# Optimization experiments

Measured on AMD Instinct MI355X. Metric: run time of the kernel, lower is better.

Reference implementation:

```python
import jax, jax.numpy as jnp
import numpy as np
from jax import lax

D_MODEL = 1024
D_STATE = 16
EXPAND = 2
KERNEL = 4
BATCH = 4
SEQ = 4096
LN_EPS = 1e-5


def _ln(x, w, b):
    m = jnp.mean(x, axis=-1, keepdims=True)
    v = jnp.mean((x - m) ** 2, axis=-1, keepdims=True)
    return (x - m) * lax.rsqrt(v + LN_EPS) * w + b


def setup_inputs() -> dict:
    key = jax.random.key(0)
    ks = jax.random.split(key, 16)
    d, n, e, k = D_MODEL, D_STATE, EXPAND, KERNEL

    def lin(key, fan_in, shape):
        bound = 1.0 / np.sqrt(fan_in)
        return jax.random.uniform(key, shape, jnp.float32, -bound, bound)

    return {
        "x": jax.random.normal(ks[0], (BATCH, SEQ, d), jnp.float32),
        "ln1_w": jnp.ones((d,), jnp.float32),
        "ln1_b": jnp.zeros((d,), jnp.float32),
        "conv_w": lin(ks[1], k, (d, 1, k)),  # depthwise conv, groups=d -> fan_in=k
        "conv_b": lin(ks[2], k, (d,)),
        "lns_w": jnp.ones((d,), jnp.float32),
        "lns_b": jnp.zeros((d,), jnp.float32),
        "in_w": lin(ks[3], d, (d, 2 * d)),
        "in_b": lin(ks[4], d, (2 * d,)),
        "xp_w": lin(ks[5], d, (d, n)),
        "xp_b": lin(ks[6], d, (n,)),
        "A_log": jax.random.normal(ks[7], (n,), jnp.float32),
        "D": jax.random.normal(ks[8], (n, d), jnp.float32),
        "out_w": lin(ks[9], d, (d, d)),
        "out_b": lin(ks[10], d, (d,)),
        "ln2_w": jnp.ones((d,), jnp.float32),
        "ln2_b": jnp.zeros((d,), jnp.float32),
        "mlp_w1": lin(ks[11], d, (d, e * d)),
        "mlp_b1": lin(ks[12], d, (e * d,)),
        "mlp_w2": lin(ks[13], e * d, (e * d, d)),
        "mlp_b2": lin(ks[14], e * d, (d,)),
    }


def reference(x, ln1_w, ln1_b, conv_w, conv_b, lns_w, lns_b, in_w, in_b,
              xp_w, xp_b, A_log, D, out_w, out_b, ln2_w, ln2_b,
              mlp_w1, mlp_b1, mlp_w2, mlp_b2):
    b, s, d = x.shape
    # --- depthwise causal-padded conv branch (truncated to seq_len) ---
    xn = _ln(x, ln1_w, ln1_b)
    xc = jnp.transpose(xn, (0, 2, 1))  # (b, d, s)
    xc = lax.conv_general_dilated(
        xc, conv_w, window_strides=(1,), padding=[(KERNEL - 1, KERNEL - 1)],
        feature_group_count=d, dimension_numbers=("NCH", "OIH", "NCH"))
    xc = xc + conv_b[None, :, None]
    xc = jnp.transpose(xc, (0, 2, 1))[:, :s]  # (b, s, d)
    x = x + xc

    # --- SelectiveScanLayer ---
    residual = x
    xn = _ln(x, lns_w, lns_b)
    xz = xn @ in_w + in_b
    xp, z = jnp.split(xz, 2, axis=-1)
    xp = jax.nn.silu(xp)
    z = jax.nn.sigmoid(z)
    u = xp @ xp_w + xp_b  # (b, s, n)
    decay = jnp.exp(-jnp.exp(A_log))  # exp(A), A = -exp(A_log); (n,)

    u_t = jnp.transpose(u, (1, 0, 2))  # (s, b, n)

    def step(h, u_i):
        h = decay * h + u_i
        return h, h

    _, hs = lax.scan(step, jnp.zeros((b, D_STATE), x.dtype), u_t)  # (s, b, n)
    ys = jnp.einsum("sbn,nd->sbd", hs, D) * jnp.transpose(z, (1, 0, 2))
    ys = ys @ out_w + out_b  # (s, b, d)
    # faithful to original: torch stack gives (1,s,b,d), then .view(b,s,d)
    y = ys.reshape(b, s, d)
    x = residual + y

    # --- MLP (dropout inactive at eval) ---
    h = _ln(x, ln2_w, ln2_b)
    h = jax.nn.gelu(h @ mlp_w1 + mlp_b1, approximate=False)
    h = h @ mlp_w2 + mlp_b2
    return x + h
```

## Files before the change

kernel.cpp:

```cpp
#include <hip/hip_runtime.h>
#include <cstdint>
#include <cstddef>


typedef short bf16x8 __attribute__((ext_vector_type(8)));
typedef float f32x4 __attribute__((ext_vector_type(4)));

#define GLD16(gp, lp)                                                          \
  __builtin_amdgcn_global_load_lds(                                            \
      (__attribute__((address_space(1))) void*)(gp),                           \
      (__attribute__((address_space(3))) void*)(lp), 16, 0, 0)

static __device__ __forceinline__ ushort f2bf(float f) {
  union { float f; uint32_t u; } c; c.f = f;
  uint32_t r = c.u + 0x7FFFu + ((c.u >> 16) & 1u);
  return (ushort)(r >> 16);
}
static __device__ __forceinline__ float bf2f(ushort u) {
  union { uint32_t u; float f; } c; c.u = ((uint32_t)u) << 16;
  return c.f;
}

template <int BF16OUT>
__global__ __launch_bounds__(256) void ln_kernel(
    const float* __restrict__ x, const float* __restrict__ w,
    const float* __restrict__ b, void* __restrict__ out) {
  const int row = blockIdx.x;
  const int tid = threadIdx.x;
  const float4 v = ((const float4*)(x + (size_t)row * 1024))[tid];
  float s  = v.x + v.y + v.z + v.w;
  float s2 = v.x * v.x + v.y * v.y + v.z * v.z + v.w * v.w;
#pragma unroll
  for (int off = 32; off > 0; off >>= 1) {
    s  += __shfl_down(s, off);
    s2 += __shfl_down(s2, off);
  }
  __shared__ float red[8];
  const int wv = tid >> 6, ln = tid & 63;
  if (ln == 0) { red[wv] = s; red[4 + wv] = s2; }
  __syncthreads();
  s  = red[0] + red[1] + red[2] + red[3];
  s2 = red[4] + red[5] + red[6] + red[7];
  const float mean = s * (1.f / 1024.f);
  const float var  = s2 * (1.f / 1024.f) - mean * mean;
  const float rstd = rsqrtf(var + 1e-5f);
  const float4 wv4 = ((const float4*)w)[tid];
  const float4 bv4 = ((const float4*)b)[tid];
  const float o0 = (v.x - mean) * rstd * wv4.x + bv4.x;
  const float o1 = (v.y - mean) * rstd * wv4.y + bv4.y;
  const float o2 = (v.z - mean) * rstd * wv4.z + bv4.z;
  const float o3 = (v.w - mean) * rstd * wv4.w + bv4.w;
  if (BF16OUT) {
    ushort4 o; o.x = f2bf(o0); o.y = f2bf(o1); o.z = f2bf(o2); o.w = f2bf(o3);
    ((ushort4*)((ushort*)out + (size_t)row * 1024))[tid] = o;
  } else {
    float4 o; o.x = o0; o.y = o1; o.z = o2; o.w = o3;
    ((float4*)((float*)out + (size_t)row * 1024))[tid] = o;
  }
}

__global__ __launch_bounds__(256) void lnconv_kernel(
    const float* __restrict__ x, const float* __restrict__ ln1w,
    const float* __restrict__ ln1b, const float* __restrict__ cw,
    const float* __restrict__ cb, const float* __restrict__ lnsw,
    const float* __restrict__ lnsb, float* __restrict__ x1,
    ushort* __restrict__ abuf) {
  const int row = blockIdx.x;
  const int t = row & 4095;
  const int tid = threadIdx.x;
  const int wv = tid >> 6, ln = tid & 63;
  const float4* x4 = (const float4*)x;
  float4 xr[4];
  float s[4], q[4];
#pragma unroll
  for (int j = 0; j < 4; j++) {
    const int tt = t - 3 + j;
    if (tt >= 0)
      xr[j] = x4[(size_t)(row - 3 + j) * 256 + tid];
    else
      xr[j] = make_float4(0.f, 0.f, 0.f, 0.f);
    s[j] = xr[j].x + xr[j].y + xr[j].z + xr[j].w;
    q[j] = xr[j].x * xr[j].x + xr[j].y * xr[j].y + xr[j].z * xr[j].z +
           xr[j].w * xr[j].w;
  }
#pragma unroll
  for (int off = 32; off > 0; off >>= 1) {
#pragma unroll
    for (int j = 0; j < 4; j++) {
      s[j] += __shfl_down(s[j], off);
      q[j] += __shfl_down(q[j], off);
    }
  }
  __shared__ float red[4][8];
  __shared__ float red2[8];
  if (ln == 0) {
#pragma unroll
    for (int j = 0; j < 4; j++) { red[wv][j] = s[j]; red[wv][4 + j] = q[j]; }
  }
  __syncthreads();
  float4 wv4 = ((const float4*)ln1w)[tid];
  float4 bv4 = ((const float4*)ln1b)[tid];
  const int c0 = tid * 4;
  float4 acc = *(const float4*)(cb + c0);
  const float4 w0 = *(const float4*)(cw + (size_t)(c0 + 0) * 4);
  const float4 w1 = *(const float4*)(cw + (size_t)(c0 + 1) * 4);
  const float4 w2 = *(const float4*)(cw + (size_t)(c0 + 2) * 4);
  const float4 w3 = *(const float4*)(cw + (size_t)(c0 + 3) * 4);
#pragma unroll
  for (int j = 0; j < 4; j++) {
    if (t - 3 + j >= 0) {
      const float sm = red[0][j] + red[1][j] + red[2][j] + red[3][j];
      const float sq = red[0][4 + j] + red[1][4 + j] + red[2][4 + j] +
                       red[3][4 + j];
      const float mean = sm * (1.f / 1024.f);
      const float var  = sq * (1.f / 1024.f) - mean * mean;
      const float rstd = rsqrtf(var + 1e-5f);
      const float lx = (xr[j].x - mean) * rstd * wv4.x + bv4.x;
      const float ly = (xr[j].y - mean) * rstd * wv4.y + bv4.y;
      const float lz = (xr[j].z - mean) * rstd * wv4.z + bv4.z;
      const float lw = (xr[j].w - mean) * rstd * wv4.w + bv4.w;
      acc.x += lx * ((const float*)&w0)[j];
      acc.y += ly * ((const float*)&w1)[j];
      acc.z += lz * ((const float*)&w2)[j];
      acc.w += lw * ((const float*)&w3)[j];
    }
  }
  float4 o;
  o.x = xr[3].x + acc.x; o.y = xr[3].y + acc.y;
  o.z = xr[3].z + acc.z; o.w = xr[3].w + acc.w;
  ((float4*)x1)[(size_t)row * 256 + tid] = o;
  float s2 = o.x + o.y + o.z + o.w;
  float q2 = o.x * o.x + o.y * o.y + o.z * o.z + o.w * o.w;
#pragma unroll
  for (int off = 32; off > 0; off >>= 1) {
    s2 += __shfl_down(s2, off);
    q2 += __shfl_down(q2, off);
  }
  if (ln == 0) { red2[wv] = s2; red2[4 + wv] = q2; }
  __syncthreads();
  const float sm = red2[0] + red2[1] + red2[2] + red2[3];
  const float sq = red2[4] + red2[5] + red2[6] + red2[7];
  const float mean = sm * (1.f / 1024.f);
  const float var  = sq * (1.f / 1024.f) - mean * mean;
  const float rstd = rsqrtf(var + 1e-5f);
  wv4 = ((const float4*)lnsw)[tid];
  bv4 = ((const float4*)lnsb)[tid];
  ushort4 a;
  a.x = f2bf((o.x - mean) * rstd * wv4.x + bv4.x);
  a.y = f2bf((o.y - mean) * rstd * wv4.y + bv4.y);
  a.z = f2bf((o.z - mean) * rstd * wv4.z + bv4.z);
  a.w = f2bf((o.w - mean) * rstd * wv4.w + bv4.w);
  ((ushort4*)(abuf + (size_t)row * 1024))[tid] = a;
}

__global__ __launch_bounds__(256) void wt_all_kernel(
    const float* __restrict__ in_w, const float* __restrict__ out_w,
    const float* __restrict__ w1, const float* __restrict__ w2,
    ushort* __restrict__ in_wT, ushort* __restrict__ out_wT,
    ushort* __restrict__ w1T, ushort* __restrict__ w2T) {
  __shared__ float tile[32][33];
  const int idx = blockIdx.x;
  const float* src; ushort* dst; int K, N, n0, k0;
  if (idx < 2048) {
    src = in_w; dst = in_wT; K = 1024; N = 2048;
    n0 = (idx & 63) * 32; k0 = (idx >> 6) * 32;
  } else if (idx < 3072) {
    const int r = idx - 2048;
    src = out_w; dst = out_wT; K = 1024; N = 1024;
    n0 = (r & 31) * 32; k0 = (r >> 5) * 32;
  } else if (idx < 5120) {
    const int r = idx - 3072;
    src = w1; dst = w1T; K = 1024; N = 2048;
    n0 = (r & 63) * 32; k0 = (r >> 6) * 32;
  } else {
    const int r = idx - 5120;
    src = w2; dst = w2T; K = 2048; N = 1024;
    n0 = (r & 31) * 32; k0 = (r >> 5) * 32;
  }
  const int tx = threadIdx.x & 31, ty = threadIdx.x >> 5;
#pragma unroll
  for (int j = 0; j < 32; j += 8)
    tile[ty + j][tx] = src[(size_t)(k0 + ty + j) * N + n0 + tx];
  __syncthreads();
#pragma unroll
  for (int j = 0; j < 32; j += 8)
    dst[(size_t)(n0 + ty + j) * K + k0 + tx] = f2bf(tile[tx][ty + j]);
}

__global__ __launch_bounds__(256) void u_mfma_kernel(
    const ushort* __restrict__ xp, const float* __restrict__ xpw,
    const float* __restrict__ xpb, float* __restrict__ u) {
  __shared__ ushort Ws[16 * 1024];
  __shared__ ushort As[64 * 64];
  const int tid = threadIdx.x;
  const int wave = tid >> 6, lane = tid & 63;
  const int l16 = lane & 15, quad = lane >> 4;
  for (int e = tid; e < 16384; e += 256) {
    const int n = e & 15, k = e >> 4;
    Ws[n * 1024 + (((k >> 3) ^ (n & 7)) << 3) + (k & 7)] =
        f2bf(xpw[(size_t)k * 16 + n]);
  }
  const int bm0 = blockIdx.x * 64;
  const int srow = lane >> 3, sblk = (lane & 7) ^ (srow & 7);
  const ushort* Ag = xp + (size_t)(bm0 + wave * 16 + srow) * 1024 + sblk * 8;
  ushort* Al = &As[wave * 16 * 64];
  const int rsw = l16 & 7;
  f32x4 acc = (f32x4){0.f, 0.f, 0.f, 0.f};
  __syncthreads();
  for (int k0 = 0; k0 < 1024; k0 += 64) {
    GLD16(Ag + k0, Al);
    GLD16(Ag + k0 + (size_t)8 * 1024, Al + 512);
    __syncthreads();
#pragma unroll
    for (int kh = 0; kh < 2; kh++) {
      const bf16x8 aF = *(const bf16x8*)
          &As[(wave * 16 + l16) * 64 + (((kh * 4 + quad) ^ rsw) << 3)];
      const bf16x8 bF = *(const bf16x8*)
          &Ws[l16 * 1024 + ((((k0 >> 3) + kh * 4 + quad) ^ rsw) << 3)];
      acc = __builtin_amdgcn_mfma_f32_16x16x32_bf16(aF, bF, acc, 0, 0, 0);
    }
    __syncthreads();
  }
  const float bv = xpb[l16];
#pragma unroll
  for (int r = 0; r < 4; r++) {
    const int row = bm0 + wave * 16 + quad * 4 + r;
    u[(size_t)row * 16 + l16] = acc[r] + bv;
  }
}

__global__ __launch_bounds__(256) void scan_kernel(
    const float* __restrict__ u, const float* __restrict__ A_log,
    float* __restrict__ hs) {
  const int tid = threadIdx.x;
  const int b = blockIdx.x >> 4;
  const int n = blockIdx.x & 15;
  const float d = expf(-expf(A_log[n]));
  const int t0 = tid * 16;
  const float* up = u + ((size_t)b * 4096) * 16 + n;
  float loc[16];
  float h = 0.f;
#pragma unroll
  for (int i = 0; i < 16; i++) {
    h = d * h + up[(size_t)(t0 + i) * 16];
    loc[i] = h;
  }
  __shared__ float sv[256];
  sv[tid] = h;
  __syncthreads();
  float d16 = d * d; d16 *= d16; d16 *= d16; d16 *= d16;
  float f = d16;
  for (int off = 1; off < 256; off <<= 1) {
    const float add = (tid >= off) ? sv[tid - off] : 0.f;
    __syncthreads();
    sv[tid] += f * add;
    __syncthreads();
    f *= f;
  }
  const float carry = (tid > 0) ? sv[tid - 1] : 0.f;
  float dp = d;
#pragma unroll
  for (int i = 0; i < 16; i++) {
    const float hg = loc[i] + dp * carry;
    dp *= d;
    hs[((size_t)(t0 + i) * 4 + b) * 16 + n] = hg;
  }
}

__global__ __launch_bounds__(256) void g_kernel(
    const float* __restrict__ hs, const float* __restrict__ Dm,
    const ushort* __restrict__ z, ushort* __restrict__ g) {
  __shared__ float hsh[256];
  const int tid = threadIdx.x;
  const int r0 = blockIdx.x * 16;
  hsh[tid] = hs[(size_t)r0 * 16 + tid];
  __syncthreads();
  float4 acc[16];
#pragma unroll
  for (int rr = 0; rr < 16; rr++) acc[rr] = make_float4(0.f, 0.f, 0.f, 0.f);
  const float4* Dv = (const float4*)Dm;
#pragma unroll
  for (int n = 0; n < 16; n++) {
    const float4 dv = Dv[(size_t)n * 256 + tid];
#pragma unroll
    for (int rr = 0; rr < 16; rr++) {
      const float h = hsh[rr * 16 + n];
      acc[rr].x += h * dv.x; acc[rr].y += h * dv.y;
      acc[rr].z += h * dv.z; acc[rr].w += h * dv.w;
    }
  }
#pragma unroll
  for (int rr = 0; rr < 16; rr++) {
    const int r = r0 + rr;
    const int b = r & 3, t = r >> 2;
    const ushort4 zv =
        *(const ushort4*)(z + ((size_t)b * 4096 + t) * 1024 + tid * 4);
    ushort4 o;
    o.x = f2bf(acc[rr].x * bf2f(zv.x)); o.y = f2bf(acc[rr].y * bf2f(zv.y));
    o.z = f2bf(acc[rr].z * bf2f(zv.z)); o.w = f2bf(acc[rr].w * bf2f(zv.w));
    *(ushort4*)(g + (size_t)r * 1024 + tid * 4) = o;
  }
}

template <int EPI>
__global__ __launch_bounds__(256) void gemm_bt(
    const ushort* __restrict__ A, const ushort* __restrict__ Bt,
    const float* __restrict__ bias, int K, void* __restrict__ p0,
    void* __restrict__ p1) {
  __shared__ ushort As[2][128 * 32];
  __shared__ ushort Bs[2][128 * 32];
  const int tid = threadIdx.x;
  const int wave = tid >> 6, lane = tid & 63;
  const int l16 = lane & 15, quad = lane >> 4;
  const int bm0 = blockIdx.x * 128, bn0 = blockIdx.y * 128;
  const int wr = (wave >> 1) * 64, wc = (wave & 1) * 64;
  const int srow = lane >> 2;
  const int skel = (((lane & 3) ^ ((srow >> 1) & 3)) << 3);

  const ushort* Ag = A + (size_t)(bm0 + wave * 32 + srow) * K + skel;
  const ushort* Bg = Bt + (size_t)(bn0 + wave * 32 + srow) * K + skel;
  const int rswz = (l16 >> 1) & 3;
  const int coff = ((quad ^ rswz) << 3);

  f32x4 acc[4][4];
#pragma unroll
  for (int i = 0; i < 4; i++)
#pragma unroll
    for (int j = 0; j < 4; j++) acc[i][j] = (f32x4){0.f, 0.f, 0.f, 0.f};

  {
    ushort* Al = &As[0][wave * 1024];
    ushort* Bl = &Bs[0][wave * 1024];
    GLD16(Ag, Al);
    GLD16(Ag + (size_t)16 * K, Al + 512);
    GLD16(Bg, Bl);
    GLD16(Bg + (size_t)16 * K, Bl + 512);
  }

  const int niter = K >> 5;
  for (int it = 0; it < niter; it++) {
    const int cur = it & 1;
    __syncthreads();
    if (it + 1 < niter) {
      const size_t k0 = (size_t)(it + 1) << 5;
      ushort* Al = &As[cur ^ 1][wave * 1024];
      ushort* Bl = &Bs[cur ^ 1][wave * 1024];
      GLD16(Ag + k0, Al);
      GLD16(Ag + k0 + (size_t)16 * K, Al + 512);
      GLD16(Bg + k0, Bl);
      GLD16(Bg + k0 + (size_t)16 * K, Bl + 512);
    }
    bf16x8 aF[4], bF[4];
#pragma unroll
    for (int i = 0; i < 4; i++)
      aF[i] = *(const bf16x8*)&As[cur][(wr + i * 16 + l16) * 32 + coff];
#pragma unroll
    for (int j = 0; j < 4; j++)
      bF[j] = *(const bf16x8*)&Bs[cur][(wc + j * 16 + l16) * 32 + coff];
#pragma unroll
    for (int i = 0; i < 4; i++)
#pragma unroll
      for (int j = 0; j < 4; j++)
        acc[i][j] = __builtin_amdgcn_mfma_f32_16x16x32_bf16(
            aF[i], bF[j], acc[i][j], 0, 0, 0);
  }

#pragma unroll
  for (int i = 0; i < 4; i++) {
    const int row0 = bm0 + wr + i * 16 + quad * 4;
#pragma unroll
    for (int j = 0; j < 4; j++) {
      const int c = bn0 + wc + j * 16 + l16;
      const float bv = bias[c];
#pragma unroll
      for (int r = 0; r < 4; r++) {
        const size_t row = (size_t)(row0 + r);
        const float v = acc[i][j][r] + bv;
        if (EPI == 0) {
          if (c < 1024)
            ((ushort*)p0)[row * 1024 + c] = f2bf(v / (1.f + __expf(-v)));
          else
            ((ushort*)p1)[row * 1024 + (c - 1024)] =
                f2bf(1.f / (1.f + __expf(-v)));
        } else if (EPI == 1) {
          float* io = (float*)p0;
          io[row * 1024 + c] += v;
        } else if (EPI == 2) {
          ((ushort*)p0)[row * 2048 + c] =
              f2bf(0.5f * v * (1.f + erff(v * 0.70710678118654752f)));
        } else {
          ((float*)p0)[row * 1024 + c] =
              ((const float*)p1)[row * 1024 + c] + v;
        }
      }
    }
  }
}

extern "C" void kernel_launch(void* const* d_in, const int* in_sizes, int n_in,
                              void* d_out, int out_size, void* d_ws,
                              size_t ws_size, hipStream_t stream) {
  const float* x      = (const float*)d_in[0];
  const float* ln1_w  = (const float*)d_in[1];
  const float* ln1_b  = (const float*)d_in[2];
  const float* conv_w = (const float*)d_in[3];
  const float* conv_b = (const float*)d_in[4];
  const float* lns_w  = (const float*)d_in[5];
  const float* lns_b  = (const float*)d_in[6];
  const float* in_w   = (const float*)d_in[7];
  const float* in_b   = (const float*)d_in[8];
  const float* xp_w   = (const float*)d_in[9];
  const float* xp_b   = (const float*)d_in[10];
  const float* A_log  = (const float*)d_in[11];
  const float* Dm     = (const float*)d_in[12];
  const float* out_w  = (const float*)d_in[13];
  const float* out_b  = (const float*)d_in[14];
  const float* ln2_w  = (const float*)d_in[15];
  const float* ln2_b  = (const float*)d_in[16];
  const float* mlp_w1 = (const float*)d_in[17];
  const float* mlp_b1 = (const float*)d_in[18];
  const float* mlp_w2 = (const float*)d_in[19];
  const float* mlp_b2 = (const float*)d_in[20];

  char* wsp = (char*)d_ws;
  size_t off = 0;
  auto alloc = [&](size_t bytes) {
    void* p = wsp + off;
    off += (bytes + 255) & ~(size_t)255;
    return p;
  };
  float*  x1    = (float*)alloc(67108864);
  ushort* abuf  = (ushort*)alloc(67108864);
  ushort* gbuf  = abuf + 16777216;
  ushort* xpb   = (ushort*)alloc(33554432);
  ushort* zb    = (ushort*)alloc(67108864);
  ushort* h1b   = (ushort*)zb;
  float*  ub    = (float*)alloc(1048576);
  float*  hsb   = (float*)alloc(1048576);
  ushort* in_wT = (ushort*)alloc(4194304);
  ushort* out_wT= (ushort*)alloc(2097152);
  ushort* w1T   = (ushort*)alloc(4194304);
  ushort* w2T   = (ushort*)alloc(4194304);

  wt_all_kernel<<<7168, 256, 0, stream>>>(in_w, out_w, mlp_w1, mlp_w2,
                                          in_wT, out_wT, w1T, w2T);
  lnconv_kernel<<<16384, 256, 0, stream>>>(x, ln1_w, ln1_b, conv_w, conv_b,
                                           lns_w, lns_b, x1, abuf);
  gemm_bt<0><<<dim3(128, 16), 256, 0, stream>>>(abuf, in_wT, in_b, 1024,
                                                xpb, zb);
  u_mfma_kernel<<<256, 256, 0, stream>>>(xpb, xp_w, xp_b, ub);
  scan_kernel<<<64, 256, 0, stream>>>(ub, A_log, hsb);
  g_kernel<<<1024, 256, 0, stream>>>(hsb, Dm, zb, gbuf);
  gemm_bt<1><<<dim3(128, 8), 256, 0, stream>>>(gbuf, out_wT, out_b, 1024,
                                               x1, nullptr);
  ln_kernel<1><<<16384, 256, 0, stream>>>(x1, ln2_w, ln2_b, xpb);
  gemm_bt<2><<<dim3(128, 16), 256, 0, stream>>>(xpb, w1T, mlp_b1, 1024,
                                                h1b, nullptr);
  gemm_bt<3><<<dim3(128, 8), 256, 0, stream>>>(h1b, w2T, mlp_b2, 2048,
                                               d_out, x1);
}
```

Baseline: 698.7 us.

## Widen GEMM N-tile to 256 and process four rows per lnconv block

The GEMM tile grows from 128x128 to 128x256, so each wave computes a 64x128 sub-tile with 32 MFMA accumulators and each A fragment is reused across twice as many B columns. Grid sizes in N are halved to match. The fused LayerNorm plus conv kernel now handles four consecutive rows per block, computing seven LN rows once instead of recomputing the three history rows for every output row. The cost is higher register pressure from 128 accumulator floats per lane, more LDS per block, fewer blocks in flight and fewer total blocks to spread across CUs.

New measurement: 890.6 us. 27.5% more time.

```diff
diff --git a/kernel.cpp b/kernel.cpp
--- a/kernel.cpp
+++ b/kernel.cpp
@@ -65,92 +65,112 @@
     const float* __restrict__ cb, const float* __restrict__ lnsw,
     const float* __restrict__ lnsb, float* __restrict__ x1,
     ushort* __restrict__ abuf) {
-  const int row = blockIdx.x;
-  const int t = row & 4095;
+  const int r0 = blockIdx.x * 4;
+  const int t0 = r0 & 4095;
   const int tid = threadIdx.x;
   const int wv = tid >> 6, ln = tid & 63;
   const float4* x4 = (const float4*)x;
-  float4 xr[4];
-  float s[4], q[4];
-#pragma unroll
-  for (int j = 0; j < 4; j++) {
-    const int tt = t - 3 + j;
-    if (tt >= 0)
-      xr[j] = x4[(size_t)(row - 3 + j) * 256 + tid];
+  float4 xr[7];
+  float s[7], q[7];
+#pragma unroll
+  for (int k = 0; k < 7; k++) {
+    if (t0 - 3 + k >= 0)
+      xr[k] = x4[(size_t)(r0 - 3 + k) * 256 + tid];
     else
-      xr[j] = make_float4(0.f, 0.f, 0.f, 0.f);
-    s[j] = xr[j].x + xr[j].y + xr[j].z + xr[j].w;
-    q[j] = xr[j].x * xr[j].x + xr[j].y * xr[j].y + xr[j].z * xr[j].z +
-           xr[j].w * xr[j].w;
+      xr[k] = make_float4(0.f, 0.f, 0.f, 0.f);
+    s[k] = xr[k].x + xr[k].y + xr[k].z + xr[k].w;
+    q[k] = xr[k].x * xr[k].x + xr[k].y * xr[k].y + xr[k].z * xr[k].z +
+           xr[k].w * xr[k].w;
   }
 #pragma unroll
   for (int off = 32; off > 0; off >>= 1) {
 #pragma unroll
-    for (int j = 0; j < 4; j++) {
-      s[j] += __shfl_down(s[j], off);
-      q[j] += __shfl_down(q[j], off);
-    }
-  }
-  __shared__ float red[4][8];
-  __shared__ float red2[8];
+    for (int k = 0; k < 7; k++) {
+      s[k] += __shfl_down(s[k], off);
+      q[k] += __shfl_down(q[k], off);
+    }
+  }
+  __shared__ float red[4][14];
+  __shared__ float red2[4][8];
   if (ln == 0) {
 #pragma unroll
-    for (int j = 0; j < 4; j++) { red[wv][j] = s[j]; red[wv][4 + j] = q[j]; }
-  }
-  __syncthreads();
-  float4 wv4 = ((const float4*)ln1w)[tid];
-  float4 bv4 = ((const float4*)ln1b)[tid];
+    for (int k = 0; k < 7; k++) { red[wv][k] = s[k]; red[wv][7 + k] = q[k]; }
+  }
+  __syncthreads();
+  const float4 w4 = ((const float4*)ln1w)[tid];
+  const float4 b4 = ((const float4*)ln1b)[tid];
+  float4 lnv[7];
+#pragma unroll
+  for (int k = 0; k < 7; k++) {
+    const float sm = red[0][k] + red[1][k] + red[2][k] + red[3][k];
+    const float sq = red[0][7 + k] + red[1][7 + k] + red[2][7 + k] +
+                     red[3][7 + k];
+    const float mean = sm * (1.f / 1024.f);
+    const float var  = sq * (1.f / 1024.f) - mean * mean;
+    const float rstd = rsqrtf(var + 1e-5f);
+    lnv[k].x = (xr[k].x - mean) * rstd * w4.x + b4.x;
+    lnv[k].y = (xr[k].y - mean) * rstd * w4.y + b4.y;
+    lnv[k].z = (xr[k].z - mean) * rstd * w4.z + b4.z;
+    lnv[k].w = (xr[k].w - mean) * rstd * w4.w + b4.w;
+  }
   const int c0 = tid * 4;
-  float4 acc = *(const float4*)(cb + c0);
+  const float4 cb4 = *(const float4*)(cb + c0);
   const float4 w0 = *(const float4*)(cw + (size_t)(c0 + 0) * 4);
   const float4 w1 = *(const float4*)(cw + (size_t)(c0 + 1) * 4);
   const float4 w2 = *(const float4*)(cw + (size_t)(c0 + 2) * 4);
   const float4 w3 = *(const float4*)(cw + (size_t)(c0 + 3) * 4);
+  float4 o[4];
+  float s2[4], q2[4];
 #pragma unroll
   for (int j = 0; j < 4; j++) {
-    if (t - 3 + j >= 0) {
-      const float sm = red[0][j] + red[1][j] + red[2][j] + red[3][j];
-      const float sq = red[0][4 + j] + red[1][4 + j] + red[2][4 + j] +
-                       red[3][4 + j];
-      const float mean = sm * (1.f / 1024.f);
-      const float var  = sq * (1.f / 1024.f) - mean * mean;
-      const float rstd = rsqrtf(var + 1e-5f);
-      const float lx = (xr[j].x - mean) * rstd * wv4.x + bv4.x;
-      const float ly = (xr[j].y - mean) * rstd * wv4.y + bv4.y;
-      const float lz = (xr[j].z - mean) * rstd * wv4.z + bv4.z;
-      const float lw = (xr[j].w - mean) * rstd * wv4.w + bv4.w;
-      acc.x += lx * ((const float*)&w0)[j];
-      acc.y += ly * ((const float*)&w1)[j];
-      acc.z += lz * ((const float*)&w2)[j];
-      acc.w += lw * ((const float*)&w3)[j];
-    }
-  }
-  float4 o;
-  o.x = xr[3].x + acc.x; o.y = xr[3].y + acc.y;
-  o.z = xr[3].z + acc.z; o.w = xr[3].w + acc.w;
-  ((float4*)x1)[(size_t)row * 256 + tid] = o;
-  float s2 = o.x + o.y + o.z + o.w;
-  float q2 = o.x * o.x + o.y * o.y + o.z * o.z + o.w * o.w;
+    float4 acc = cb4;
+#pragma unroll
+    for (int jj = 0; jj < 4; jj++) {
+      if (t0 + j - 3 + jj >= 0) {
+        const float4 lv = lnv[j + jj];
+        acc.x += lv.x * ((const float*)&w0)[jj];
+        acc.y += lv.y * ((const float*)&w1)[jj];
+        acc.z += lv.z * ((const float*)&w2)[jj];
+        acc.w += lv.w * ((const float*)&w3)[jj];
+      }
+    }
+    o[j].x = xr[3 + j].x + acc.x; o[j].y = xr[3 + j].y + acc.y;
+    o[j].z = xr[3 + j].z + acc.z; o[j].w = xr[3 + j].w + acc.w;
+    ((float4*)x1)[(size_t)(r0 + j) * 256 + tid] = o[j];
+    s2[j] = o[j].x + o[j].y + o[j].z + o[j].w;
+    q2[j] = o[j].x * o[j].x + o[j].y * o[j].y + o[j].z * o[j].z +
+            o[j].w * o[j].w;
+  }
 #pragma unroll
   for (int off = 32; off > 0; off >>= 1) {
-    s2 += __shfl_down(s2, off);
-    q2 += __shfl_down(q2, off);
-  }
-  if (ln == 0) { red2[wv] = s2; red2[4 + wv] = q2; }
-  __syncthreads();
-  const float sm = red2[0] + red2[1] + red2[2] + red2[3];
-  const float sq = red2[4] + red2[5] + red2[6] + red2[7];
-  const float mean = sm * (1.f / 1024.f);
-  const float var  = sq * (1.f / 1024.f) - mean * mean;
-  const float rstd = rsqrtf(var + 1e-5f);
-  wv4 = ((const float4*)lnsw)[tid];
-  bv4 = ((const float4*)lnsb)[tid];
-  ushort4 a;
-  a.x = f2bf((o.x - mean) * rstd * wv4.x + bv4.x);
-  a.y = f2bf((o.y - mean) * rstd * wv4.y + bv4.y);
-  a.z = f2bf((o.z - mean) * rstd * wv4.z + bv4.z);
-  a.w = f2bf((o.w - mean) * rstd * wv4.w + bv4.w);
-  ((ushort4*)(abuf + (size_t)row * 1024))[tid] = a;
+#pragma unroll
+    for (int j = 0; j < 4; j++) {
+      s2[j] += __shfl_down(s2[j], off);
+      q2[j] += __shfl_down(q2[j], off);
+    }
+  }
+  if (ln == 0) {
+#pragma unroll
+    for (int j = 0; j < 4; j++) { red2[wv][j] = s2[j]; red2[wv][4 + j] = q2[j]; }
+  }
+  __syncthreads();
+  const float4 ws4 = ((const float4*)lnsw)[tid];
+  const float4 bs4 = ((const float4*)lnsb)[tid];
+#pragma unroll
+  for (int j = 0; j < 4; j++) {
+    const float sm = red2[0][j] + red2[1][j] + red2[2][j] + red2[3][j];
+    const float sq = red2[0][4 + j] + red2[1][4 + j] + red2[2][4 + j] +
+                     red2[3][4 + j];
+    const float mean = sm * (1.f / 1024.f);
+    const float var  = sq * (1.f / 1024.f) - mean * mean;
+    const float rstd = rsqrtf(var + 1e-5f);
+    ushort4 a;
+    a.x = f2bf((o[j].x - mean) * rstd * ws4.x + bs4.x);
+    a.y = f2bf((o[j].y - mean) * rstd * ws4.y + bs4.y);
+    a.z = f2bf((o[j].z - mean) * rstd * ws4.z + bs4.z);
+    a.w = f2bf((o[j].w - mean) * rstd * ws4.w + bs4.w);
+    ((ushort4*)(abuf + (size_t)(r0 + j) * 1024))[tid] = a;
+  }
 }
 
 __global__ __launch_bounds__(256) void wt_all_kernel(
@@ -308,33 +328,34 @@
     const float* __restrict__ bias, int K, void* __restrict__ p0,
     void* __restrict__ p1) {
   __shared__ ushort As[2][128 * 32];
-  __shared__ ushort Bs[2][128 * 32];
+  __shared__ ushort Bs[2][256 * 32];
   const int tid = threadIdx.x;
   const int wave = tid >> 6, lane = tid & 63;
   const int l16 = lane & 15, quad = lane >> 4;
-  const int bm0 = blockIdx.x * 128, bn0 = blockIdx.y * 128;
-  const int wr = (wave >> 1) * 64, wc = (wave & 1) * 64;
+  const int bm0 = blockIdx.x * 128, bn0 = blockIdx.y * 256;
+  const int wr = (wave >> 1) * 64, wc = (wave & 1) * 128;
   const int srow = lane >> 2;
   const int skel = (((lane & 3) ^ ((srow >> 1) & 3)) << 3);
 
   const ushort* Ag = A + (size_t)(bm0 + wave * 32 + srow) * K + skel;
-  const ushort* Bg = Bt + (size_t)(bn0 + wave * 32 + srow) * K + skel;
+  const ushort* Bg = Bt + (size_t)(bn0 + wave * 64 + srow) * K + skel;
   const int rswz = (l16 >> 1) & 3;
   const int coff = ((quad ^ rswz) << 3);
 
-  f32x4 acc[4][4];
+  f32x4 acc[4][8];
 #pragma unroll
   for (int i = 0; i < 4; i++)
 #pragma unroll
-    for (int j = 0; j < 4; j++) acc[i][j] = (f32x4){0.f, 0.f, 0.f, 0.f};
+    for (int j = 0; j < 8; j++) acc[i][j] = (f32x4){0.f, 0.f, 0.f, 0.f};
 
   {
     ushort* Al = &As[0][wave * 1024];
-    ushort* Bl = &Bs[0][wave * 1024];
+    ushort* Bl = &Bs[0][wave * 2048];
     GLD16(Ag, Al);
     GLD16(Ag + (size_t)16 * K, Al + 512);
-    GLD16(Bg, Bl);
-    GLD16(Bg + (size_t)16 * K, Bl + 512);
+#pragma unroll
+    for (int rb = 0; rb < 4; rb++)
+      GLD16(Bg + (size_t)(16 * rb) * K, Bl + rb * 512);
   }
 
   const int niter = K >> 5;
@@ -344,23 +365,24 @@
     if (it + 1 < niter) {
       const size_t k0 = (size_t)(it + 1) << 5;
       ushort* Al = &As[cur ^ 1][wave * 1024];
-      ushort* Bl = &Bs[cur ^ 1][wave * 1024];
+      ushort* Bl = &Bs[cur ^ 1][wave * 2048];
       GLD16(Ag + k0, Al);
       GLD16(Ag + k0 + (size_t)16 * K, Al + 512);
-      GLD16(Bg + k0, Bl);
-      GLD16(Bg + k0 + (size_t)16 * K, Bl + 512);
-    }
-    bf16x8 aF[4], bF[4];
+#pragma unroll
+      for (int rb = 0; rb < 4; rb++)
+        GLD16(Bg + k0 + (size_t)(16 * rb) * K, Bl + rb * 512);
+    }
+    bf16x8 aF[4], bF[8];
 #pragma unroll
     for (int i = 0; i < 4; i++)
       aF[i] = *(const bf16x8*)&As[cur][(wr + i * 16 + l16) * 32 + coff];
 #pragma unroll
-    for (int j = 0; j < 4; j++)
+    for (int j = 0; j < 8; j++)
       bF[j] = *(const bf16x8*)&Bs[cur][(wc + j * 16 + l16) * 32 + coff];
 #pragma unroll
     for (int i = 0; i < 4; i++)
 #pragma unroll
-      for (int j = 0; j < 4; j++)
+      for (int j = 0; j < 8; j++)
         acc[i][j] = __builtin_amdgcn_mfma_f32_16x16x32_bf16(
             aF[i], bF[j], acc[i][j], 0, 0, 0);
   }
@@ -369,7 +391,7 @@
   for (int i = 0; i < 4; i++) {
     const int row0 = bm0 + wr + i * 16 + quad * 4;
 #pragma unroll
-    for (int j = 0; j < 4; j++) {
+    for (int j = 0; j < 8; j++) {
       const int c = bn0 + wc + j * 16 + l16;
       const float bv = bias[c];
 #pragma unroll
@@ -444,18 +466,18 @@
 
   wt_all_kernel<<<7168, 256, 0, stream>>>(in_w, out_w, mlp_w1, mlp_w2,
                                           in_wT, out_wT, w1T, w2T);
-  lnconv_kernel<<<16384, 256, 0, stream>>>(x, ln1_w, ln1_b, conv_w, conv_b,
-                                           lns_w, lns_b, x1, abuf);
-  gemm_bt<0><<<dim3(128, 16), 256, 0, stream>>>(abuf, in_wT, in_b, 1024,
-                                                xpb, zb);
+  lnconv_kernel<<<4096, 256, 0, stream>>>(x, ln1_w, ln1_b, conv_w, conv_b,
+                                          lns_w, lns_b, x1, abuf);
+  gemm_bt<0><<<dim3(128, 8), 256, 0, stream>>>(abuf, in_wT, in_b, 1024,
+                                               xpb, zb);
   u_mfma_kernel<<<256, 256, 0, stream>>>(xpb, xp_w, xp_b, ub);
   scan_kernel<<<64, 256, 0, stream>>>(ub, A_log, hsb);
   g_kernel<<<1024, 256, 0, stream>>>(hsb, Dm, zb, gbuf);
-  gemm_bt<1><<<dim3(128, 8), 256, 0, stream>>>(gbuf, out_wT, out_b, 1024,
+  gemm_bt<1><<<dim3(128, 4), 256, 0, stream>>>(gbuf, out_wT, out_b, 1024,
                                                x1, nullptr);
   ln_kernel<1><<<16384, 256, 0, stream>>>(x1, ln2_w, ln2_b, xpb);
-  gemm_bt<2><<<dim3(128, 16), 256, 0, stream>>>(xpb, w1T, mlp_b1, 1024,
-                                                h1b, nullptr);
-  gemm_bt<3><<<dim3(128, 8), 256, 0, stream>>>(h1b, w2T, mlp_b2, 2048,
+  gemm_bt<2><<<dim3(128, 8), 256, 0, stream>>>(xpb, w1T, mlp_b1, 1024,
+                                               h1b, nullptr);
+  gemm_bt<3><<<dim3(128, 4), 256, 0, stream>>>(h1b, w2T, mlp_b2, 2048,
                                                d_out, x1);
 }
```
